# Kernel tuning notes

Hardware: AMD Instinct MI355X
Metric: run time of the kernel (lower is better)

The kernel has to match this reference:

```python
import jax, jax.numpy as jnp
import numpy as np

D_STATE = 16
D_CONV = 4
DT_RANK = 2  # ceil(d_model/16) with d_model=32


def _conv2d(x, w, b, pad, dil=1, groups=1):
    y = jax.lax.conv_general_dilated(
        x, w, (1, 1), ((pad, pad), (pad, pad)), rhs_dilation=(dil, dil),
        feature_group_count=groups, dimension_numbers=('NCHW', 'OIHW', 'NCHW'))
    return y + b[None, :, None, None]


def _ssm(xc, delta, A, Bc, Cc, D):
    # xc,delta: (B,L,Di); A: (Di,N); Bc,Cc: (B,L,N)
    dA = jnp.exp(delta[..., None] * A)                       # (B,L,Di,N)
    dBx = delta[..., None] * Bc[:, :, None, :] * xc[..., None]
    def comb(e1, e2):
        a1, b1 = e1
        a2, b2 = e2
        return a2 * a1, a2 * b1 + b2
    _, h = jax.lax.associative_scan(comb, (dA, dBx), axis=1)  # h_t = dA_t*h_{t-1}+dBx_t
    return jnp.einsum('bldn,bln->bld', h, Cc) + xc * D


def _dir(xin, cw, cb, wx, wdt, bdt, A_log, D):
    # causal depthwise conv1d over L, then silu
    L = xin.shape[1]
    xp = jnp.pad(xin, ((0, 0), (D_CONV - 1, 0), (0, 0)))
    xc = sum(xp[:, k:k + L, :] * cw[:, k] for k in range(D_CONV)) + cb
    xc = jax.nn.silu(xc)
    dbc = xc @ wx.T                                          # (B,L,dt_rank+2N)
    dt, Bc, Cc = jnp.split(dbc, [DT_RANK, DT_RANK + D_STATE], axis=-1)
    delta = jax.nn.softplus(dt @ wdt.T + bdt)
    return _ssm(xc, delta, -jnp.exp(A_log), Bc, Cc, D)


def _mamba(xn, w_in, cwf, cbf, wxf, wdtf, bdtf, Af, Df,
           cwb, cbb, wxb, wdtb, bdtb, Ab, Db, w_out):
    xz = xn @ w_in.T                                         # (B,L,2*Di)
    xin, z = jnp.split(xz, 2, axis=-1)
    y_f = _dir(xin, cwf, cbf, wxf, wdtf, bdtf, Af, Df)
    y_b = jnp.flip(_dir(jnp.flip(xin, axis=1), cwb, cbb, wxb, wdtb, bdtb, Ab, Db), axis=1)
    return ((y_f + y_b) * jax.nn.silu(z)) @ w_out.T          # bimamba v2: sum of directions


def _forward(x, w_att, b_att, ln_w, ln_b, w_in,
             conv_w_f, conv_b_f, wx_f, wdt_f, bdt_f, A_log_f, D_f,
             conv_w_b, conv_b_b, wx_b, wdt_b, bdt_b, A_log_b, D_b,
             w_out, w_se, b_se, w_conv, b_conv):
    B, C, H, W = x.shape
    att1 = x
    xa = _conv2d(x, w_att, b_att, pad=9, dil=3, groups=C)    # dilated depthwise, same HxW
    xf = xa.reshape(B, C, H * W).transpose(0, 2, 1)          # (B,L,C)
    mu = xf.mean(-1, keepdims=True)
    var = xf.var(-1, keepdims=True)
    xn = (xf - mu) / jnp.sqrt(var + 1e-5) * ln_w + ln_b
    out = _mamba(xn, w_in, conv_w_f, conv_b_f, wx_f, wdt_f, bdt_f, A_log_f, D_f,
                 conv_w_b, conv_b_b, wx_b, wdt_b, bdt_b, A_log_b, D_b, w_out)
    att2 = out.transpose(0, 2, 1).reshape(B, C, H, W)
    att = jnp.concatenate([att1, att2], axis=1)
    pooled = jnp.concatenate([att.mean(1, keepdims=True), att.max(1, keepdims=True)], axis=1)
    se = jax.nn.sigmoid(_conv2d(pooled, w_se, b_se, pad=3))
    output = att1 * se[:, 0:1] + att2 * se[:, 1:2]
    return _conv2d(output, w_conv, b_conv, pad=1)


def setup_inputs() -> dict:
    key = jax.random.key(0)
    ks = jax.random.split(key, 16)
    B, C, H, W = 4, 32, 96, 96
    Di, OUT = 64, 64
    n = jax.random.normal
    A_log = jnp.tile(jnp.log(jnp.arange(1, D_STATE + 1, dtype=jnp.float32)), (Di, 1))
    return {
        'x': n(ks[0], (B, C, H, W), jnp.float32),
        'w_att': n(ks[1], (C, 1, 7, 7), jnp.float32) * 0.05,
        'b_att': jnp.zeros((C,), jnp.float32),
        'ln_w': jnp.ones((C,), jnp.float32),
        'ln_b': jnp.zeros((C,), jnp.float32),
        'w_in': n(ks[2], (2 * Di, C), jnp.float32) / np.sqrt(C),
        'conv_w_f': n(ks[3], (Di, D_CONV), jnp.float32) * 0.3,
        'conv_b_f': jnp.zeros((Di,), jnp.float32),
        'wx_f': n(ks[4], (DT_RANK + 2 * D_STATE, Di), jnp.float32) / np.sqrt(Di),
        'wdt_f': n(ks[5], (Di, DT_RANK), jnp.float32) * 0.5,
        'bdt_f': n(ks[6], (Di,), jnp.float32) * 0.1,
        'A_log_f': A_log,
        'D_f': jnp.ones((Di,), jnp.float32),
        'conv_w_b': n(ks[7], (Di, D_CONV), jnp.float32) * 0.3,
        'conv_b_b': jnp.zeros((Di,), jnp.float32),
        'wx_b': n(ks[8], (DT_RANK + 2 * D_STATE, Di), jnp.float32) / np.sqrt(Di),
        'wdt_b': n(ks[9], (Di, DT_RANK), jnp.float32) * 0.5,
        'bdt_b': n(ks[10], (Di,), jnp.float32) * 0.1,
        'A_log_b': A_log,
        'D_b': jnp.ones((Di,), jnp.float32),
        'w_out': n(ks[11], (C, Di), jnp.float32) / np.sqrt(Di),
        'w_se': n(ks[12], (2, 2, 7, 7), jnp.float32) * 0.1,
        'b_se': jnp.zeros((2,), jnp.float32),
        'w_conv': n(ks[13], (OUT, C, 3, 3), jnp.float32) * 0.06,
        'b_conv': jnp.zeros((OUT,), jnp.float32),
    }


def reference(x, w_att, b_att, ln_w, ln_b, w_in,
              conv_w_f, conv_b_f, wx_f, wdt_f, bdt_f, A_log_f, D_f,
              conv_w_b, conv_b_b, wx_b, wdt_b, bdt_b, A_log_b, D_b,
              w_out, w_se, b_se, w_conv, b_conv):
    return _forward(x, w_att, b_att, ln_w, ln_b, w_in,
                    conv_w_f, conv_b_f, wx_f, wdt_f, bdt_f, A_log_f, D_f,
                    conv_w_b, conv_b_b, wx_b, wdt_b, bdt_b, A_log_b, D_b,
                    w_out, w_se, b_se, w_conv, b_conv)
```

## Files before the change

### kernel.cpp

```cpp
#include <hip/hip_runtime.h>
#include <math.h>

#define BB 4
#define CH 32
#define HH 96
#define WW 96
#define LL (HH*WW)
#define DI 64
#define NS 16
#define BL (BB*LL)
#define NCH 144
#define CLEN (LL/NCH)

__device__ __forceinline__ float sigmoidf_(float x){ return 1.f/(1.f+__expf(-x)); }
__device__ __forceinline__ float siluf_(float x){ return x*sigmoidf_(x); }
__device__ __forceinline__ float softplusf_(float x){
  return (x > 15.f) ? x : __logf(1.f + __expf(x));
}
#define WAVE_LDS_FENCE() do { asm volatile("s_waitcnt lgkmcnt(0)" ::: "memory"); __builtin_amdgcn_sched_barrier(0); } while(0)

__global__ __launch_bounds__(256) void k1_conv_att(
    const float* __restrict__ x, const float* __restrict__ w,
    const float* __restrict__ bias, float* __restrict__ xa){
  int idx = blockIdx.x*256 + threadIdx.x;
  if (idx >= BB*CH*LL) return;
  int w0 = idx % WW; int h0 = (idx/WW) % HH; int c = (idx/LL) % CH;
  const float* xp = x + (idx/LL)*LL;
  const float* wp = w + c*49;
  float acc = bias[c];
  #pragma unroll
  for (int kh=0; kh<7; ++kh){
    int hh = h0 + 3*kh - 9;
    if ((unsigned)hh >= HH) continue;
    const float* row = xp + hh*WW;
    #pragma unroll
    for (int kw=0; kw<7; ++kw){
      int ww = w0 + 3*kw - 9;
      if ((unsigned)ww < WW) acc += row[ww]*wp[kh*7+kw];
    }
  }
  xa[idx] = acc;
}

__global__ __launch_bounds__(128) void k2_ln_inproj(
    const float* __restrict__ xa, const float* __restrict__ w_in,
    const float* __restrict__ ln_w, const float* __restrict__ ln_b,
    float* __restrict__ xin, float* __restrict__ zs){
  __shared__ float xs[CH*65];
  __shared__ float wl[128*33];
  __shared__ float smu[64], srs[64];
  int tid = threadIdx.x;
  int tg0 = blockIdx.x*64;
  int bb = tg0 / LL;
  int l0 = tg0 % LL;
  const float* xab = xa + bb*CH*LL + l0;
  for (int r=0; r<16; ++r){
    int idx = r*128 + tid;
    int c = idx >> 6, t = idx & 63;
    xs[c*65+t] = xab[c*LL + t];
  }
  for (int r=0; r<32; ++r){
    int idx = r*128 + tid;
    int j = idx >> 5, c = idx & 31;
    wl[j*33+c] = ln_w[c]*w_in[idx];
  }
  __syncthreads();
  if (tid < 64){
    float s=0.f, s2=0.f;
    #pragma unroll
    for (int c=0;c<CH;++c){ float v = xs[c*65+tid]; s+=v; s2+=v*v; }
    float mu = s*(1.f/CH);
    float var = s2*(1.f/CH) - mu*mu;
    smu[tid]=mu; srs[tid]=rsqrtf(var+1e-5f);
  }
  int j = tid;
  float swl=0.f, bj=0.f;
  #pragma unroll
  for (int c=0;c<CH;++c){ swl += wl[j*33+c]; bj += ln_b[c]*w_in[j*32+c]; }
  __syncthreads();
  for (int t=0;t<64;++t){
    float acc=0.f;
    #pragma unroll
    for (int c=0;c<CH;++c) acc += xs[c*65+t]*wl[j*33+c];
    float out = srs[t]*(acc - smu[t]*swl) + bj;
    int base = ((bb*LL) + l0 + t)*DI;
    if (j < DI) xin[base + j] = out;
    else        zs[base + (j-DI)] = siluf_(out);
  }
}

__global__ __launch_bounds__(64) void k3_fused(
    const float* __restrict__ xin,
    const float* __restrict__ cw_f, const float* __restrict__ cb_f,
    const float* __restrict__ wx_f, const float* __restrict__ wdt_f, const float* __restrict__ bdt_f,
    const float* __restrict__ Al_f,
    const float* __restrict__ cw_b, const float* __restrict__ cb_b,
    const float* __restrict__ wx_b, const float* __restrict__ wdt_b, const float* __restrict__ bdt_b,
    const float* __restrict__ Al_b,
    float* __restrict__ xc_f, float* __restrict__ dl_f, float* __restrict__ Bc_f, float* __restrict__ Cc_f,
    float* __restrict__ xc_b, float* __restrict__ dl_b, float* __restrict__ Bc_b, float* __restrict__ Cc_b,
    float* __restrict__ aggP, float* __restrict__ aggS){
  int lane = threadIdx.x;
  int dir = blockIdx.y;
  int bb = blockIdx.z;
  int ch = blockIdx.x;
  int p0 = ch*CLEN;
  const float* cw  = dir? cw_b : cw_f;
  const float* cb  = dir? cb_b : cb_f;
  const float* wx  = dir? wx_b : wx_f;
  const float* wdt = dir? wdt_b : wdt_f;
  const float* bdt = dir? bdt_b : bdt_f;
  const float* Al  = dir? Al_b : Al_f;
  float* xcbuf = dir? xc_b : xc_f;
  float* dlbuf = dir? dl_b : dl_f;
  float* Bcb   = dir? Bc_b : Bc_f;
  float* Ccb   = dir? Cc_b : Cc_f;

  __shared__ float xcs[64];
  __shared__ float bcs[16];
  __shared__ float dtb[2];

  int d = lane;
  float c0=cw[d*4+0], c1=cw[d*4+1], c2=cw[d*4+2], c3=cw[d*4+3], cbv=cb[d];
  float wd0=wdt[d*2], wd1=wdt[d*2+1], bd=bdt[d];
  float A[NS];
  #pragma unroll
  for (int n4=0;n4<4;++n4){
    float4 av = *(const float4*)&Al[d*NS + n4*4];
    A[n4*4+0] = -__expf(av.x); A[n4*4+1] = -__expf(av.y);
    A[n4*4+2] = -__expf(av.z); A[n4*4+3] = -__expf(av.w);
  }
  float wreg[64];
  if (lane < 34){
    #pragma unroll
    for (int c4=0;c4<16;++c4){
      float4 wv = *(const float4*)&wx[lane*64 + c4*4];
      wreg[c4*4+0]=wv.x; wreg[c4*4+1]=wv.y; wreg[c4*4+2]=wv.z; wreg[c4*4+3]=wv.w;
    }
  }
  float P[NS], S[NS];
  #pragma unroll
  for (int n=0;n<NS;++n){ P[n]=1.f; S[n]=0.f; }
  float u1=0.f,u2=0.f,u3=0.f;
  #pragma unroll
  for (int k=1;k<=3;++k){
    int pos = p0 - k;
    float v = 0.f;
    if (pos >= 0){ int ls = dir? (LL-1-pos) : pos; v = xin[(bb*LL+ls)*DI + d]; }
    if(k==1) u1=v; else if(k==2) u2=v; else u3=v;
  }

  for (int t=0;t<CLEN;++t){
    int pos = p0 + t;
    int ls = dir? (LL-1-pos) : pos;
    int tb = bb*LL + pos;
    float u0 = xin[(bb*LL+ls)*DI + d];
    float xc = siluf_(cbv + c0*u3 + c1*u2 + c2*u1 + c3*u0);
    u3=u2; u2=u1; u1=u0;
    xcbuf[tb*DI + d] = xc;
    xcs[d] = xc;
    WAVE_LDS_FENCE();
    if (lane < 34){
      float acc = 0.f;
      #pragma unroll
      for (int c4=0;c4<16;++c4){
        float4 xv = *(const float4*)&xcs[c4*4];
        acc += xv.x*wreg[c4*4+0] + xv.y*wreg[c4*4+1]
             + xv.z*wreg[c4*4+2] + xv.w*wreg[c4*4+3];
      }
      if (lane < 2){
        dtb[lane] = acc;
      } else if (lane < 18){
        Bcb[tb*NS + lane-2] = acc;
        bcs[lane-2] = acc;
      } else {
        Ccb[tb*NS + lane-18] = acc;
      }
    }
    WAVE_LDS_FENCE();
    float dt0 = dtb[0], dt1 = dtb[1];
    float dlt = softplusf_(dt0*wd0 + dt1*wd1 + bd);
    dlbuf[tb*DI + d] = dlt;
    float dx = dlt*xc;
    #pragma unroll
    for (int n4=0;n4<4;++n4){
      float4 bv = *(const float4*)&bcs[n4*4];
      float bvv[4] = {bv.x,bv.y,bv.z,bv.w};
      #pragma unroll
      for (int j=0;j<4;++j){
        int n = n4*4+j;
        float dA = __expf(dlt*A[n]);
        P[n] *= dA;
        S[n] = dA*S[n] + dx*bvv[j];
      }
    }
  }
  int bdd = (bb*2+dir)*DI + d;
  float* pp = aggP + (bdd*NCH + ch)*NS;
  float* sp = aggS + (bdd*NCH + ch)*NS;
  #pragma unroll
  for (int n4=0;n4<4;++n4){
    *(float4*)&pp[n4*4] = make_float4(P[n4*4+0],P[n4*4+1],P[n4*4+2],P[n4*4+3]);
    *(float4*)&sp[n4*4] = make_float4(S[n4*4+0],S[n4*4+1],S[n4*4+2],S[n4*4+3]);
  }
}

__global__ __launch_bounds__(256) void p2_scan_agg(
    const float* aggP, const float* aggS, float* hin){
  int t = blockIdx.x*256 + threadIdx.x;
  if (t >= BB*2*DI*NS) return;
  int bdd = t >> 4, n = t & 15;
  float h = 0.f;
  for (int k=0;k<NCH;++k){
    int i = (bdd*NCH + k)*NS + n;
    float pv = aggP[i], sv = aggS[i];
    hin[i] = h;
    h = pv*h + sv;
  }
}

__global__ __launch_bounds__(64) void p3_scan_out(
    const float* __restrict__ dl_f, const float* __restrict__ xc_f,
    const float* __restrict__ Bc_f, const float* __restrict__ Cc_f,
    const float* __restrict__ dl_b, const float* __restrict__ xc_b,
    const float* __restrict__ Bc_b, const float* __restrict__ Cc_b,
    const float* __restrict__ Al_f, const float* __restrict__ D_f,
    const float* __restrict__ Al_b, const float* __restrict__ D_b,
    const float* __restrict__ hin, float* __restrict__ y_f, float* __restrict__ y_b){
  int lane = threadIdx.x;
  int dir = blockIdx.y >> 1;
  int dhalf = blockIdx.y & 1;
  int bb = blockIdx.z; int ch = blockIdx.x;
  int d = dhalf*32 + (lane & 31);
  int nb = (lane >> 5) * 8;
  const float* dl = dir? dl_b : dl_f;
  const float* xc = dir? xc_b : xc_f;
  const float* Bc = dir? Bc_b : Bc_f;
  const float* Cc = dir? Cc_b : Cc_f;
  const float* Al = dir? Al_b : Al_f;
  const float* Dv = dir? D_b : D_f;
  float* y = dir? y_b : y_f;
  float A[8];
  #pragma unroll
  for (int n4=0;n4<2;++n4){
    float4 av = *(const float4*)&Al[d*NS + nb + n4*4];
    A[n4*4+0] = -__expf(av.x); A[n4*4+1] = -__expf(av.y);
    A[n4*4+2] = -__expf(av.z); A[n4*4+3] = -__expf(av.w);
  }
  float Dd = Dv[d];
  int bdd = (bb*2+dir)*DI + d;
  const float* hp = hin + (bdd*NCH + ch)*NS + nb;
  float h[8];
  #pragma unroll
  for (int n4=0;n4<2;++n4){
    float4 hv = *(const float4*)&hp[n4*4];
    h[n4*4+0]=hv.x; h[n4*4+1]=hv.y; h[n4*4+2]=hv.z; h[n4*4+3]=hv.w;
  }
  int p0 = ch*CLEN;
  for (int t=0;t<CLEN;++t){
    int tb = bb*LL + p0 + t;
    float dlt = dl[tb*DI+d];
    float xcv = xc[tb*DI+d];
    float dx = dlt*xcv;
    float acc = 0.f;
    #pragma unroll
    for (int n4=0;n4<2;++n4){
      float4 bv = *(const float4*)&Bc[tb*NS + nb + n4*4];
      float4 cv = *(const float4*)&Cc[tb*NS + nb + n4*4];
      float bvv[4]={bv.x,bv.y,bv.z,bv.w}, cvv[4]={cv.x,cv.y,cv.z,cv.w};
      #pragma unroll
      for (int j=0;j<4;++j){
        int n = n4*4+j;
        float dA = __expf(dlt*A[n]);
        h[n] = dA*h[n] + dx*bvv[j];
        acc += h[n]*cvv[j];
      }
    }
    float other = __shfl_xor(acc, 32, 64);
    if (lane < 32) y[tb*DI + d] = xcv*Dd + acc + other;
  }
}

__global__ __launch_bounds__(256) void k4_outproj(
    const float* __restrict__ y_f, const float* __restrict__ y_b, const float* __restrict__ zs,
    const float* __restrict__ w_out, float* __restrict__ att2){
  __shared__ float gt[64*64];
  __shared__ float wol[32*65];
  __shared__ float ot[32*65];
  int tid = threadIdx.x;
  int tg0 = blockIdx.x*64;
  int bb = tg0/LL, l0 = tg0%LL;
  for (int r=0;r<8;++r){
    int idx = r*256+tid;
    wol[(idx>>6)*65 + (idx&63)] = w_out[idx];
  }
  for (int r=0;r<16;++r){
    int idx = r*256+tid;
    int tk = idx>>6, d = idx&63;
    int l = l0+tk;
    int tbf = (bb*LL + l)*DI + d;
    int tbb = (bb*LL + (LL-1-l))*DI + d;
    gt[idx] = (y_f[tbf] + y_b[tbb]) * zs[tbf];
  }
  __syncthreads();
  int c = tid & 31, tsl = tid >> 5;
  for (int tg=0; tg<8; ++tg){
    int tk = tg*8+tsl;
    float acc=0.f;
    #pragma unroll
    for (int d=0;d<DI;++d) acc += gt[tk*64+d]*wol[c*65+d];
    ot[c*65+tk] = acc;
  }
  __syncthreads();
  float* a2 = att2 + bb*CH*LL + l0;
  for (int r=0;r<8;++r){
    int idx = r*256+tid;
    int cc2 = idx>>6, t = idx&63;
    a2[cc2*LL + t] = ot[cc2*65+t];
  }
}

__global__ __launch_bounds__(256) void k5a_pool(
    const float* __restrict__ x, const float* __restrict__ att2, float* __restrict__ pooled){
  int idx = blockIdx.x*256+threadIdx.x;
  if (idx>=BL) return;
  int bb = idx/LL, l = idx%LL;
  const float* xp = x + bb*CH*LL + l;
  const float* ap = att2 + bb*CH*LL + l;
  float s=0.f, m=-INFINITY;
  for (int c=0;c<CH;++c){
    float v1 = xp[c*LL], v2 = ap[c*LL];
    s += v1+v2;
    m = fmaxf(m, fmaxf(v1,v2));
  }
  pooled[(bb*2+0)*LL + l] = s*(1.f/64.f);
  pooled[(bb*2+1)*LL + l] = m;
}

__global__ __launch_bounds__(256) void k5b_se_combine(
    const float* __restrict__ x, const float* __restrict__ att2,
    const float* __restrict__ pooled, const float* __restrict__ w_se,
    const float* __restrict__ b_se, float* __restrict__ outbuf){
  int idx = blockIdx.x*256+threadIdx.x;
  if (idx>=BL) return;
  int bb = idx/LL, l = idx%LL;
  int h0 = l/WW, w0 = l%WW;
  float a0 = b_se[0], a1 = b_se[1];
  #pragma unroll
  for (int i=0;i<2;++i){
    const float* pp = pooled + (bb*2+i)*LL;
    for (int kh=0;kh<7;++kh){
      int hh = h0+kh-3; if((unsigned)hh>=HH) continue;
      for (int kw=0;kw<7;++kw){
        int ww2 = w0+kw-3; if((unsigned)ww2>=WW) continue;
        float v = pp[hh*WW+ww2];
        a0 += v*w_se[(i*7+kh)*7+kw];
        a1 += v*w_se[((2+i)*7+kh)*7+kw];
      }
    }
  }
  float se0 = sigmoidf_(a0), se1 = sigmoidf_(a1);
  const float* xp = x + bb*CH*LL + l;
  const float* ap = att2 + bb*CH*LL + l;
  float* op = outbuf + bb*CH*LL + l;
  for (int c=0;c<CH;++c) op[c*LL] = xp[c*LL]*se0 + ap[c*LL]*se1;
}

__global__ __launch_bounds__(256) void k6_conv3x3(
    const float* __restrict__ inb, const float* __restrict__ wc,
    const float* __restrict__ bc, float* __restrict__ out){
  __shared__ float lds[CH*3*98];
  int tid = threadIdx.x;
  int h = blockIdx.x, cohalf = blockIdx.y, bb = blockIdx.z;
  const float* ib = inb + bb*CH*LL;
  for (int r=0; r<36; ++r){
    int idx = r*256+tid;
    int ci = idx/(3*96); int rr = (idx/96)%3; int ww2 = idx%96;
    int hh = h + rr - 1;
    float v = ((unsigned)hh < HH) ? ib[ci*LL + hh*WW + ww2] : 0.f;
    lds[(ci*3+rr)*98 + 1 + ww2] = v;
  }
  if (tid < 96){
    int ci = tid/3, rr = tid%3;
    lds[(ci*3+rr)*98 + 0]  = 0.f;
    lds[(ci*3+rr)*98 + 97] = 0.f;
  }
  __syncthreads();
  int coslot = tid >> 4, wslot = tid & 15;
  int co0 = cohalf*32 + coslot*2, wb = wslot*6;
  float acc[2][6];
  #pragma unroll
  for (int q=0;q<2;++q)
    #pragma unroll
    for (int j2=0;j2<6;++j2) acc[q][j2]=0.f;
  for (int ci=0; ci<CH; ++ci){
    float wt[2][9];
    #pragma unroll
    for (int q=0;q<2;++q){
      const float* wp = wc + ((co0+q)*CH + ci)*9;
      #pragma unroll
      for (int k=0;k<9;++k) wt[q][k] = wp[k];
    }
    #pragma unroll
    for (int kh=0;kh<3;++kh){
      const float* row = &lds[(ci*3+kh)*98 + wb];
      float s[8];
      #pragma unroll
      for (int t2=0;t2<8;++t2) s[t2] = row[t2];
      #pragma unroll
      for (int q=0;q<2;++q)
        #pragma unroll
        for (int kw=0;kw<3;++kw){
          float wv = wt[q][kh*3+kw];
          #pragma unroll
          for (int j2=0;j2<6;++j2) acc[q][j2] += s[j2+kw]*wv;
        }
    }
  }
  #pragma unroll
  for (int q=0;q<2;++q){
    int co = co0+q;
    float bv = bc[co];
    float* op = out + (bb*64 + co)*LL + h*WW + wb;
    #pragma unroll
    for (int j2=0;j2<6;++j2) op[j2] = acc[q][j2]+bv;
  }
}

extern "C" void kernel_launch(void* const* d_in, const int* in_sizes, int n_in,
                              void* d_out, int out_size, void* d_ws, size_t ws_size,
                              hipStream_t stream){
  const float* x     = (const float*)d_in[0];
  const float* w_att = (const float*)d_in[1];
  const float* b_att = (const float*)d_in[2];
  const float* ln_w  = (const float*)d_in[3];
  const float* ln_b  = (const float*)d_in[4];
  const float* w_in  = (const float*)d_in[5];
  const float* cw_f  = (const float*)d_in[6];
  const float* cb_f  = (const float*)d_in[7];
  const float* wx_f  = (const float*)d_in[8];
  const float* wdt_f = (const float*)d_in[9];
  const float* bdt_f = (const float*)d_in[10];
  const float* Al_f  = (const float*)d_in[11];
  const float* D_f   = (const float*)d_in[12];
  const float* cw_b  = (const float*)d_in[13];
  const float* cb_b  = (const float*)d_in[14];
  const float* wx_b  = (const float*)d_in[15];
  const float* wdt_b = (const float*)d_in[16];
  const float* bdt_b = (const float*)d_in[17];
  const float* Al_b  = (const float*)d_in[18];
  const float* D_b   = (const float*)d_in[19];
  const float* w_out = (const float*)d_in[20];
  const float* w_se  = (const float*)d_in[21];
  const float* b_se  = (const float*)d_in[22];
  const float* w_conv= (const float*)d_in[23];
  const float* b_conv= (const float*)d_in[24];

  float* ws = (float*)d_ws;
  float* xa     = ws + 0;
  float* att2   = ws + 0;
  float* xin    = ws + 1179648;
  float* outbuf = ws + 1179648;
  float* pooled = ws + 2359296;
  float* zs     = ws + 3538944;
  float* xc_f   = ws + 5898240;
  float* xc_b   = ws + 8257536;
  float* dl_f   = ws + 10616832;
  float* dl_b   = ws + 12976128;
  float* Bc_f   = ws + 15335424;
  float* Bc_b   = ws + 15925248;
  float* Cc_f   = ws + 16515072;
  float* Cc_b   = ws + 17104896;
  float* y_f    = ws + 17694720;
  float* y_b    = ws + 20054016;
  float* aggP   = ws + 22413312;
  float* aggS   = ws + 23592960;
  float* hin    = aggP;

  k1_conv_att<<<4608,256,0,stream>>>(x, w_att, b_att, xa);
  k2_ln_inproj<<<576,128,0,stream>>>(xa, w_in, ln_w, ln_b, xin, zs);
  k3_fused<<<dim3(NCH,2,BB),64,0,stream>>>(xin,
      cw_f,cb_f,wx_f,wdt_f,bdt_f,Al_f, cw_b,cb_b,wx_b,wdt_b,bdt_b,Al_b,
      xc_f,dl_f,Bc_f,Cc_f, xc_b,dl_b,Bc_b,Cc_b, aggP,aggS);
  p2_scan_agg<<<32,256,0,stream>>>(aggP,aggS,hin);
  p3_scan_out<<<dim3(NCH,4,BB),64,0,stream>>>(dl_f,xc_f,Bc_f,Cc_f, dl_b,xc_b,Bc_b,Cc_b,
      Al_f,D_f, Al_b,D_b, hin, y_f,y_b);
  k4_outproj<<<576,256,0,stream>>>(y_f,y_b,zs,w_out,att2);
  k5a_pool<<<144,256,0,stream>>>(x, att2, pooled);
  k5b_se_combine<<<144,256,0,stream>>>(x, att2, pooled, w_se, b_se, outbuf);
  k6_conv3x3<<<dim3(HH,2,BB),256,0,stream>>>(outbuf, w_conv, b_conv, (float*)d_out);
}
```

Measured before the change: 367.5 us.

## Batch k3 timesteps in groups, register-cache in_proj weights, tweak scan kernels

k3_fused now computes the conv/silu and the x_proj dot products for eight timesteps per LDS fence pair instead of one, which cuts per-step synchronisation overhead. k2 keeps each thread's LN-scaled in_proj weights in registers and reads x via float4 over four timesteps, dropping the weight LDS tile. p2 gets restrict qualifiers and partial unrolling, and p3 splits its C-reduction into four partial sums with the time loop unrolled by two. hin moves out of aggP into the dead xin region so it no longer aliases the scan inputs. Register pressure in k3 rises with the xcr array on top of the existing 64-float wreg.

```diff
diff --git a/kernel.cpp b/kernel.cpp
--- a/kernel.cpp
+++ b/kernel.cpp
@@ -11,6 +11,7 @@
 #define BL (BB*LL)
 #define NCH 144
 #define CLEN (LL/NCH)
+#define GG 8
 
 __device__ __forceinline__ float sigmoidf_(float x){ return 1.f/(1.f+__expf(-x)); }
 __device__ __forceinline__ float siluf_(float x){ return x*sigmoidf_(x); }
@@ -46,8 +47,7 @@
     const float* __restrict__ xa, const float* __restrict__ w_in,
     const float* __restrict__ ln_w, const float* __restrict__ ln_b,
     float* __restrict__ xin, float* __restrict__ zs){
-  __shared__ float xs[CH*65];
-  __shared__ float wl[128*33];
+  __shared__ float xs[CH*68];
   __shared__ float smu[64], srs[64];
   int tid = threadIdx.x;
   int tg0 = blockIdx.x*64;
@@ -57,35 +57,44 @@
   for (int r=0; r<16; ++r){
     int idx = r*128 + tid;
     int c = idx >> 6, t = idx & 63;
-    xs[c*65+t] = xab[c*LL + t];
-  }
-  for (int r=0; r<32; ++r){
-    int idx = r*128 + tid;
-    int j = idx >> 5, c = idx & 31;
-    wl[j*33+c] = ln_w[c]*w_in[idx];
+    xs[c*68+t] = xab[c*LL + t];
+  }
+  int j = tid;
+  float wlj[CH];
+  float swl=0.f, bj=0.f;
+  #pragma unroll
+  for (int c=0;c<CH;++c){
+    float wv = ln_w[c]*w_in[j*CH+c];
+    wlj[c] = wv; swl += wv;
+    bj += ln_b[c]*w_in[j*CH+c];
   }
   __syncthreads();
   if (tid < 64){
     float s=0.f, s2=0.f;
     #pragma unroll
-    for (int c=0;c<CH;++c){ float v = xs[c*65+tid]; s+=v; s2+=v*v; }
+    for (int c=0;c<CH;++c){ float v = xs[c*68+tid]; s+=v; s2+=v*v; }
     float mu = s*(1.f/CH);
     float var = s2*(1.f/CH) - mu*mu;
     smu[tid]=mu; srs[tid]=rsqrtf(var+1e-5f);
   }
-  int j = tid;
-  float swl=0.f, bj=0.f;
-  #pragma unroll
-  for (int c=0;c<CH;++c){ swl += wl[j*33+c]; bj += ln_b[c]*w_in[j*32+c]; }
   __syncthreads();
-  for (int t=0;t<64;++t){
-    float acc=0.f;
-    #pragma unroll
-    for (int c=0;c<CH;++c) acc += xs[c*65+t]*wl[j*33+c];
-    float out = srs[t]*(acc - smu[t]*swl) + bj;
-    int base = ((bb*LL) + l0 + t)*DI;
-    if (j < DI) xin[base + j] = out;
-    else        zs[base + (j-DI)] = siluf_(out);
+  for (int t4=0;t4<16;++t4){
+    float a0=0.f,a1=0.f,a2=0.f,a3=0.f;
+    #pragma unroll
+    for (int c=0;c<CH;++c){
+      float4 xv = *(const float4*)&xs[c*68 + t4*4];
+      float wv = wlj[c];
+      a0 += xv.x*wv; a1 += xv.y*wv; a2 += xv.z*wv; a3 += xv.w*wv;
+    }
+    float av[4] = {a0,a1,a2,a3};
+    #pragma unroll
+    for (int q=0;q<4;++q){
+      int t = t4*4+q;
+      float out = srs[t]*(av[q] - smu[t]*swl) + bj;
+      int base = ((bb*LL) + l0 + t)*DI;
+      if (j < DI) xin[base + j] = out;
+      else        zs[base + (j-DI)] = siluf_(out);
+    }
   }
 }
 
@@ -116,9 +125,9 @@
   float* Bcb   = dir? Bc_b : Bc_f;
   float* Ccb   = dir? Cc_b : Cc_f;
 
-  __shared__ float xcs[64];
-  __shared__ float bcs[16];
-  __shared__ float dtb[2];
+  __shared__ float xcs[GG*64];
+  __shared__ float bcs[GG*16];
+  __shared__ float dtb[GG*2];
 
   int d = lane;
   float c0=cw[d*4+0], c1=cw[d*4+1], c2=cw[d*4+2], c3=cw[d*4+3], cbv=cb[d];
@@ -150,48 +159,61 @@
     if(k==1) u1=v; else if(k==2) u2=v; else u3=v;
   }
 
-  for (int t=0;t<CLEN;++t){
-    int pos = p0 + t;
-    int ls = dir? (LL-1-pos) : pos;
-    int tb = bb*LL + pos;
-    float u0 = xin[(bb*LL+ls)*DI + d];
-    float xc = siluf_(cbv + c0*u3 + c1*u2 + c2*u1 + c3*u0);
-    u3=u2; u2=u1; u1=u0;
-    xcbuf[tb*DI + d] = xc;
-    xcs[d] = xc;
+  for (int g=0; g<CLEN/GG; ++g){
+    int pbase = p0 + g*GG;
+    float xcr[GG];
+    #pragma unroll
+    for (int j=0;j<GG;++j){
+      int pos = pbase + j;
+      int ls = dir? (LL-1-pos) : pos;
+      float u0 = xin[(bb*LL+ls)*DI + d];
+      float xc = siluf_(cbv + c0*u3 + c1*u2 + c2*u1 + c3*u0);
+      u3=u2; u2=u1; u1=u0;
+      xcr[j] = xc;
+      xcs[j*64+d] = xc;
+    }
+    #pragma unroll
+    for (int j=0;j<GG;++j) xcbuf[(bb*LL+pbase+j)*DI + d] = xcr[j];
     WAVE_LDS_FENCE();
     if (lane < 34){
-      float acc = 0.f;
       #pragma unroll
-      for (int c4=0;c4<16;++c4){
-        float4 xv = *(const float4*)&xcs[c4*4];
-        acc += xv.x*wreg[c4*4+0] + xv.y*wreg[c4*4+1]
-             + xv.z*wreg[c4*4+2] + xv.w*wreg[c4*4+3];
+      for (int j=0;j<GG;++j){
+        float acc = 0.f;
+        #pragma unroll
+        for (int c4=0;c4<16;++c4){
+          float4 xv = *(const float4*)&xcs[j*64 + c4*4];
+          acc += xv.x*wreg[c4*4+0] + xv.y*wreg[c4*4+1]
+               + xv.z*wreg[c4*4+2] + xv.w*wreg[c4*4+3];
+        }
+        int tb = bb*LL + pbase + j;
+        if (lane < 2){
+          dtb[j*2+lane] = acc;
+        } else if (lane < 18){
+          Bcb[tb*NS + lane-2] = acc;
+          bcs[j*16 + lane-2] = acc;
+        } else {
+          Ccb[tb*NS + lane-18] = acc;
+        }
       }
-      if (lane < 2){
-        dtb[lane] = acc;
-      } else if (lane < 18){
-        Bcb[tb*NS + lane-2] = acc;
-        bcs[lane-2] = acc;
-      } else {
-        Ccb[tb*NS + lane-18] = acc;
-      }
     }
     WAVE_LDS_FENCE();
-    float dt0 = dtb[0], dt1 = dtb[1];
-    float dlt = softplusf_(dt0*wd0 + dt1*wd1 + bd);
-    dlbuf[tb*DI + d] = dlt;
-    float dx = dlt*xc;
-    #pragma unroll
-    for (int n4=0;n4<4;++n4){
-      float4 bv = *(const float4*)&bcs[n4*4];
-      float bvv[4] = {bv.x,bv.y,bv.z,bv.w};
+    #pragma unroll
+    for (int j=0;j<GG;++j){
+      int tb = bb*LL + pbase + j;
+      float dlt = softplusf_(dtb[j*2]*wd0 + dtb[j*2+1]*wd1 + bd);
+      dlbuf[tb*DI + d] = dlt;
+      float dx = dlt*xcr[j];
       #pragma unroll
-      for (int j=0;j<4;++j){
-        int n = n4*4+j;
-        float dA = __expf(dlt*A[n]);
-        P[n] *= dA;
-        S[n] = dA*S[n] + dx*bvv[j];
+      for (int n4=0;n4<4;++n4){
+        float4 bv = *(const float4*)&bcs[j*16 + n4*4];
+        float bvv[4] = {bv.x,bv.y,bv.z,bv.w};
+        #pragma unroll
+        for (int q=0;q<4;++q){
+          int n = n4*4+q;
+          float dA = __expf(dlt*A[n]);
+          P[n] *= dA;
+          S[n] = dA*S[n] + dx*bvv[q];
+        }
       }
     }
   }
@@ -206,11 +228,13 @@
 }
 
 __global__ __launch_bounds__(256) void p2_scan_agg(
-    const float* aggP, const float* aggS, float* hin){
+    const float* __restrict__ aggP, const float* __restrict__ aggS,
+    float* __restrict__ hin){
   int t = blockIdx.x*256 + threadIdx.x;
   if (t >= BB*2*DI*NS) return;
   int bdd = t >> 4, n = t & 15;
   float h = 0.f;
+  #pragma unroll 4
   for (int k=0;k<NCH;++k){
     int i = (bdd*NCH + k)*NS + n;
     float pv = aggP[i], sv = aggS[i];
@@ -257,25 +281,26 @@
     h[n4*4+0]=hv.x; h[n4*4+1]=hv.y; h[n4*4+2]=hv.z; h[n4*4+3]=hv.w;
   }
   int p0 = ch*CLEN;
+  #pragma unroll 2
   for (int t=0;t<CLEN;++t){
     int tb = bb*LL + p0 + t;
     float dlt = dl[tb*DI+d];
     float xcv = xc[tb*DI+d];
     float dx = dlt*xcv;
-    float acc = 0.f;
-    #pragma unroll
-    for (int n4=0;n4<2;++n4){
-      float4 bv = *(const float4*)&Bc[tb*NS + nb + n4*4];
-      float4 cv = *(const float4*)&Cc[tb*NS + nb + n4*4];
-      float bvv[4]={bv.x,bv.y,bv.z,bv.w}, cvv[4]={cv.x,cv.y,cv.z,cv.w};
-      #pragma unroll
-      for (int j=0;j<4;++j){
-        int n = n4*4+j;
-        float dA = __expf(dlt*A[n]);
-        h[n] = dA*h[n] + dx*bvv[j];
-        acc += h[n]*cvv[j];
-      }
-    }
+    float4 bv0 = *(const float4*)&Bc[tb*NS + nb];
+    float4 bv1 = *(const float4*)&Bc[tb*NS + nb + 4];
+    float4 cv0 = *(const float4*)&Cc[tb*NS + nb];
+    float4 cv1 = *(const float4*)&Cc[tb*NS + nb + 4];
+    float bvv[8]={bv0.x,bv0.y,bv0.z,bv0.w,bv1.x,bv1.y,bv1.z,bv1.w};
+    float cvv[8]={cv0.x,cv0.y,cv0.z,cv0.w,cv1.x,cv1.y,cv1.z,cv1.w};
+    float pacc[4]={0.f,0.f,0.f,0.f};
+    #pragma unroll
+    for (int n=0;n<8;++n){
+      float dA = __expf(dlt*A[n]);
+      h[n] = dA*h[n] + dx*bvv[n];
+      pacc[n&3] += h[n]*cvv[n];
+    }
+    float acc = (pacc[0]+pacc[1]) + (pacc[2]+pacc[3]);
     float other = __shfl_xor(acc, 32, 64);
     if (lane < 32) y[tb*DI + d] = xcv*Dd + acc + other;
   }
@@ -460,6 +485,7 @@
   float* xa     = ws + 0;
   float* att2   = ws + 0;
   float* xin    = ws + 1179648;
+  float* hin    = ws + 1179648;
   float* outbuf = ws + 1179648;
   float* pooled = ws + 2359296;
   float* zs     = ws + 3538944;
@@ -475,7 +501,6 @@
   float* y_b    = ws + 20054016;
   float* aggP   = ws + 22413312;
   float* aggS   = ws + 23592960;
-  float* hin    = aggP;
 
   k1_conv_att<<<4608,256,0,stream>>>(x, w_att, b_att, xa);
   k2_ln_inproj<<<576,128,0,stream>>>(xa, w_in, ln_w, ln_b, xin, zs);
```

After: 370.3 us. Within noise of the previous version (+0.8%).
